# Kernel tuning notes

Measured on AMD Instinct MI355X. Metric: run time of the kernel, lower is better.

Reference implementation:

```python
import jax, jax.numpy as jnp
import numpy as np

N_HEAD = 16
D_MODEL = 1024
D_HEAD = D_MODEL // N_HEAD
B, T = 2, 2048


def setup_inputs() -> dict:
    key = jax.random.key(0)
    k1, k2, k3 = jax.random.split(key, 3)
    x = jax.random.normal(k1, (B, T, D_MODEL), dtype=jnp.float32)
    w_attn = jax.random.normal(k2, (3 * D_MODEL, D_MODEL), dtype=jnp.float32) * (D_MODEL ** -0.5)
    w_proj = jax.random.normal(k3, (D_MODEL, D_MODEL), dtype=jnp.float32) * (D_MODEL ** -0.5)
    return {"x": x, "w_attn": w_attn, "w_proj": w_proj}


def _rms_norm(x):
    eps = jnp.asarray(jnp.finfo(x.dtype).eps, x.dtype)
    var = jnp.mean(jnp.square(x), axis=-1, keepdims=True)
    return x * jax.lax.rsqrt(var + eps)


def _rotate_half(x):
    x1, x2 = jnp.split(x, 2, axis=-1)
    return jnp.concatenate((-x2, x1), axis=-1)


def reference(x, w_attn, w_proj):
    Bx, Tx, C = x.shape
    qkv = jnp.einsum('btc,fc->btf', x, w_attn)  # [B,T,3C]
    q, k, v = jnp.split(qkv, 3, axis=-1)
    # [B, H, T, Dh]
    q = q.reshape(Bx, Tx, N_HEAD, D_HEAD).transpose(0, 2, 1, 3)
    k = k.reshape(Bx, Tx, N_HEAD, D_HEAD).transpose(0, 2, 1, 3)
    v = v.reshape(Bx, Tx, N_HEAD, D_HEAD).transpose(0, 2, 1, 3)
    # QK RMSNorm (no learned weight)
    q = _rms_norm(q)
    k = _rms_norm(k)
    # Rotary embedding over full d_head: freqs tiled twice
    inv_freq = 1.0 / (10000.0 ** (jnp.arange(0, D_HEAD, 2, dtype=jnp.float32) / D_HEAD))
    t = jnp.arange(Tx, dtype=jnp.float32)
    freqs = jnp.einsum('i,j->ij', t, inv_freq)  # [T, Dh/2]
    emb = jnp.concatenate((freqs, freqs), axis=-1)  # [T, Dh]
    cos = jnp.cos(emb)[None, None, :, :]
    sin = jnp.sin(emb)[None, None, :, :]
    q = q * cos + _rotate_half(q) * sin
    k = k * cos + _rotate_half(k) * sin
    # Causal SDPA
    scale = D_HEAD ** -0.5
    scores = jnp.einsum('bhqd,bhkd->bhqk', q, k) * scale
    causal = jnp.tril(jnp.ones((Tx, Tx), dtype=bool))
    scores = jnp.where(causal[None, None], scores, jnp.asarray(-jnp.inf, scores.dtype))
    attn = jax.nn.softmax(scores, axis=-1)
    y = jnp.einsum('bhqk,bhkd->bhqd', attn, v)
    y = y.transpose(0, 2, 1, 3).reshape(Bx, Tx, C)
    return jnp.einsum('btc,oc->bto', y, w_proj)
```

## Files before the change

kernel.cpp:

```cpp
#include <hip/hip_runtime.h>
#include <cstdint>
#include <cstddef>


typedef short bf16x8 __attribute__((ext_vector_type(8)));
typedef float floatx4 __attribute__((ext_vector_type(4)));
typedef unsigned short ushortx8 __attribute__((ext_vector_type(8)));
typedef unsigned short ushortx4 __attribute__((ext_vector_type(4)));
typedef unsigned int uintx2 __attribute__((ext_vector_type(2)));

#define DEVI __device__ __forceinline__

DEVI float bf2f(unsigned short u) {
    unsigned int x = ((unsigned int)u) << 16;
    return __builtin_bit_cast(float, x);
}
DEVI unsigned short f2bf(float f) {
    unsigned int u = __builtin_bit_cast(unsigned int, f);
    u += 0x7fffu + ((u >> 16) & 1u);
    return (unsigned short)(u >> 16);
}
DEVI unsigned int pkbf2(float a, float b) {
    unsigned int ua = __builtin_bit_cast(unsigned int, a) + 0x8000u;
    unsigned int ub = __builtin_bit_cast(unsigned int, b) + 0x8000u;
    return __builtin_amdgcn_perm(ub, ua, 0x07060302);
}

DEVI void glds16(const unsigned short* g, unsigned short* l) {
    __builtin_amdgcn_global_load_lds(
        (const __attribute__((address_space(1))) unsigned int*)g,
        (__attribute__((address_space(3))) unsigned int*)l, 16, 0, 0);
}

DEVI void cast8(unsigned short* dst, const float* src) {
    floatx4 a = *(const floatx4*)src;
    floatx4 b = *(const floatx4*)(src + 4);
    ushortx8 o;
    o[0] = f2bf(a[0]); o[1] = f2bf(a[1]); o[2] = f2bf(a[2]); o[3] = f2bf(a[3]);
    o[4] = f2bf(b[0]); o[5] = f2bf(b[1]); o[6] = f2bf(b[2]); o[7] = f2bf(b[3]);
    *(ushortx8*)dst = o;
}

__global__ __launch_bounds__(256)
void cast_inputs(const float* __restrict__ x, const float* __restrict__ wa,
                 const float* __restrict__ wp,
                 unsigned short* __restrict__ xb, unsigned short* __restrict__ wab,
                 unsigned short* __restrict__ wpb)
{
    size_t g = (size_t)blockIdx.x * 256 + threadIdx.x;
    size_t stride = (size_t)gridDim.x * 256;
    for (size_t i = g; i < (4194304 / 8); i += stride) cast8(xb  + i * 8, x  + i * 8);
    for (size_t i = g; i < (3145728 / 8); i += stride) cast8(wab + i * 8, wa + i * 8);
    for (size_t i = g; i < (1048576 / 8); i += stride) cast8(wpb + i * 8, wp + i * 8);
}

template <bool QKV_SPLIT, int BN, int BK>
__global__ __launch_bounds__(256)
void gemm_bt(const unsigned short* __restrict__ A, const unsigned short* __restrict__ B,
             unsigned short* __restrict__ Cqk, float* __restrict__ Cf,
             unsigned short* __restrict__ Vt, int M, int N, int K)
{
    constexpr int WCOLS = (BN == 128) ? 2 : 1;
    constexpr int WROWS = 4 / WCOLS;
    constexpr int MI    = 128 / (16 * WROWS);
    constexpr int LPR   = BK / 8;
    constexpr int RPI   = 64 / LPR;

    __shared__ __align__(16) unsigned short As[128 * BK];
    __shared__ __align__(16) unsigned short Bs[BN * BK];

    const int tid  = threadIdx.x;
    const int lane = tid & 63;
    const int w    = tid >> 6;
    const int wm   = w / WCOLS, wn = w % WCOLS;
    const int quad = lane >> 4;
    const int lm   = lane & 15;
    const int m0 = blockIdx.y * 128;
    const int n0 = blockIdx.x * BN;
    const int sr = lane / LPR;
    const int sc = (lane % LPR) * 8;

    floatx4 acc[MI][4] = {};

    for (int k0 = 0; k0 < K; k0 += BK) {
        __syncthreads();
        #pragma unroll
        for (int i = 0; i < 32 / RPI; ++i) {
            int r = w * 32 + i * RPI;
            glds16(&A[(size_t)(m0 + r + sr) * K + k0 + sc], &As[r * BK]);
        }
        #pragma unroll
        for (int i = 0; i < (BN / 4) / RPI; ++i) {
            int r = w * (BN / 4) + i * RPI;
            glds16(&B[(size_t)(n0 + r + sr) * K + k0 + sc], &Bs[r * BK]);
        }
        __syncthreads();

        #pragma unroll
        for (int kk = 0; kk < BK / 32; ++kk) {
            bf16x8 a[MI];
            #pragma unroll
            for (int i = 0; i < MI; ++i)
                a[i] = *(const bf16x8*)&As[(wm * (16 * MI) + i * 16 + lm) * BK + kk * 32 + quad * 8];
            #pragma unroll
            for (int j = 0; j < 4; ++j) {
                bf16x8 b = *(const bf16x8*)&Bs[(wn * 64 + j * 16 + lm) * BK + kk * 32 + quad * 8];
                #pragma unroll
                for (int i = 0; i < MI; ++i)
                    acc[i][j] = __builtin_amdgcn_mfma_f32_16x16x32_bf16(a[i], b, acc[i][j], 0, 0, 0);
            }
        }
    }

    if constexpr (QKV_SPLIT) {
        const bool is_v = (n0 + wn * 64) >= 2048;
        if (!is_v) {
            float rn[MI][4];
            #pragma unroll
            for (int i = 0; i < MI; ++i)
                #pragma unroll
                for (int r = 0; r < 4; ++r) {
                    float s = 0.0f;
                    #pragma unroll
                    for (int j = 0; j < 4; ++j) s += acc[i][j][r] * acc[i][j][r];
                    s += __shfl_xor(s, 1, 64);
                    s += __shfl_xor(s, 2, 64);
                    s += __shfl_xor(s, 4, 64);
                    s += __shfl_xor(s, 8, 64);
                    rn[i][r] = rsqrtf(s * (1.0f / 64.0f) + 1.1920929e-07f);
                }
            float invf[4];
            #pragma unroll
            for (int j = 0; j < 4; ++j) {
                int d = j * 16 + lm;
                invf[j] = __expf(-(float)(d & 31) * 0.28782313662425572f);
            }
            #pragma unroll
            for (int i = 0; i < MI; ++i)
                #pragma unroll
                for (int r = 0; r < 4; ++r) {
                    int row = m0 + wm * (16 * MI) + i * 16 + quad * 4 + r;
                    float t = (float)(row & 2047);
                    float g = rn[i][r];
                    #pragma unroll
                    for (int j = 0; j < 4; ++j) {
                        int d = j * 16 + lm;
                        float sn, cs;
                        __sincosf(t * invf[j], &sn, &cs);
                        float v  = acc[i][j][r] * g;
                        float vp = acc[i][j ^ 2][r] * g;
                        float sgn = (d < 32) ? -1.0f : 1.0f;
                        Cqk[(size_t)row * 2048 + (n0 + wn * 64 + d)] =
                            f2bf(v * cs + sgn * vp * sn);
                    }
                }
        } else {
            #pragma unroll
            for (int i = 0; i < MI; ++i)
                #pragma unroll
                for (int j = 0; j < 4; ++j) {
                    int col  = n0 + wn * 64 + j * 16 + lm;
                    int row0 = m0 + wm * (16 * MI) + i * 16 + quad * 4;
                    int bq = row0 >> 11, t0 = row0 & 2047;
                    ushortx4 pk;
                    #pragma unroll
                    for (int r = 0; r < 4; ++r) pk[r] = f2bf(acc[i][j][r]);
                    *(ushortx4*)&Vt[((size_t)(bq * 1024 + (col - 2048))) * 2048 + t0] = pk;
                }
        }
    } else {
        #pragma unroll
        for (int i = 0; i < MI; ++i)
            #pragma unroll
            for (int j = 0; j < 4; ++j) {
                int col  = n0 + wn * 64 + j * 16 + lm;
                int row0 = m0 + wm * (16 * MI) + i * 16 + quad * 4;
                #pragma unroll
                for (int r = 0; r < 4; ++r)
                    Cf[(size_t)(row0 + r) * N + col] = acc[i][j][r];
            }
    }
}

#define ATTN_STEP(KSc, VSc, KSn, VSn, KT, DG, LAST)                            \
  do {                                                                         \
    if (!(LAST)) {                                                             \
      *(ushortx8*)&(KSn)[r0 * LD + pc] = kreg0;                                \
      *(ushortx8*)&(KSn)[r1 * LD + pc] = kreg1;                                \
      *(ushortx8*)&(VSn)[r0 * LD + pc] = vreg0;                                \
      *(ushortx8*)&(VSn)[r1 * LD + pc] = vreg1;                                \
      if ((KT) + 2 <= qt) {                                                    \
        kreg0 = *(const ushortx8*)kp0; kreg1 = *(const ushortx8*)kp1;          \
        vreg0 = *(const ushortx8*)vp0; vreg1 = *(const ushortx8*)vp1;          \
        kp0 += (size_t)64 * 2048; kp1 += (size_t)64 * 2048;                    \
        vp0 += 64; vp1 += 64;                                                  \
      }                                                                        \
    }                                                                          \
    floatx4 sa[4] = {};                                                        \
    _Pragma("unroll")                                                          \
    for (int kk = 0; kk < 2; ++kk)                                             \
      _Pragma("unroll")                                                        \
      for (int j = 0; j < 4; ++j) {                                            \
        bf16x8 kf = *(const bf16x8*)&(KSc)[(j * 16 + lm) * LD + kk * 32 + quad * 8]; \
        sa[j] = __builtin_amdgcn_mfma_f32_16x16x32_bf16(kf, qf[kk], sa[j], 0, 0, 0); \
      }                                                                        \
    _Pragma("unroll")                                                          \
    for (int j = 0; j < 4; ++j) {                                              \
      float p0 = exp2f(sa[j][0] * c1 - c2);                                    \
      float p1 = exp2f(sa[j][1] * c1 - c2);                                    \
      float p2 = exp2f(sa[j][2] * c1 - c2);                                    \
      float p3 = exp2f(sa[j][3] * c1 - c2);                                    \
      if (DG) {                                                                \
        int kb = (KT) * 64 + j * 16 + quad * 4;                                \
        if (kb + 0 > qrow) p0 = 0.0f;                                          \
        if (kb + 1 > qrow) p1 = 0.0f;                                          \
        if (kb + 2 > qrow) p2 = 0.0f;                                          \
        if (kb + 3 > qrow) p3 = 0.0f;                                          \
      }                                                                        \
      uintx2 pk;                                                               \
      pk[0] = pkbf2(p0, p1);                                                   \
      pk[1] = pkbf2(p2, p3);                                                   \
      *(uintx2*)&QPs[(w * 16 + lm) * LD + j * 16 + quad * 4] = pk;             \
    }                                                                          \
    _Pragma("unroll")                                                          \
    for (int kk = 0; kk < 2; ++kk) {                                           \
      bf16x8 pf = *(const bf16x8*)&QPs[(w * 16 + lm) * LD + kk * 32 + quad * 8]; \
      _Pragma("unroll")                                                        \
      for (int j = 0; j < 4; ++j) {                                            \
        bf16x8 vf = *(const bf16x8*)&(VSc)[(j * 16 + lm) * LD + kk * 32 + quad * 8]; \
        o[j] = __builtin_amdgcn_mfma_f32_16x16x32_bf16(pf, vf, o[j], 0, 0, 0); \
      }                                                                        \
      l_acc = __builtin_amdgcn_mfma_f32_16x16x32_bf16(pf, ones, l_acc, 0, 0, 0); \
    }                                                                          \
    if (!(LAST)) __syncthreads();                                              \
  } while (0)

__global__ __launch_bounds__(256)
void attention(const unsigned short* __restrict__ qk,
               const unsigned short* __restrict__ Vt,
               unsigned short* __restrict__ Y)
{
    constexpr int LD = 72;
    __shared__ __align__(16) unsigned short QPs[64 * LD];
    __shared__ __align__(16) unsigned short Ks0[64 * LD];
    __shared__ __align__(16) unsigned short Ks1[64 * LD];
    __shared__ __align__(16) unsigned short Vs0[64 * LD];
    __shared__ __align__(16) unsigned short Vs1[64 * LD];

    const int tid  = threadIdx.x;
    const int lane = tid & 63;
    const int w    = tid >> 6;
    const int quad = lane >> 4;
    const int lm   = lane & 15;

    const int bh = blockIdx.x;
    const int qt = 31 - blockIdx.y;
    const int b  = bh >> 4, h = bh & 15;
    const int q0 = qt * 64;
    const int qrow = q0 + w * 16 + lm;

    const int r0 = tid >> 3, r1 = r0 + 32, pc = (tid & 7) * 8;
    const unsigned short* kp0 = qk + (size_t)b * 2048 * 2048 + 1024 + h * 64
                              + (size_t)r0 * 2048 + pc;
    const unsigned short* kp1 = kp0 + (size_t)32 * 2048;
    const unsigned short* vp0 = Vt + (size_t)bh * 64 * 2048 + (size_t)r0 * 2048 + pc;
    const unsigned short* vp1 = vp0 + (size_t)32 * 2048;

    #pragma unroll
    for (int i = 0; i < 2; ++i) {
        int c = i * 256 + tid, row = c >> 3, col = (c & 7) * 8;
        *(ushortx8*)&QPs[row * LD + col] =
            *(const ushortx8*)&qk[((size_t)(b * 2048 + q0 + row)) * 2048 + h * 64 + col];
    }

    ushortx8 kreg0 = *(const ushortx8*)kp0, kreg1 = *(const ushortx8*)kp1;
    ushortx8 vreg0 = *(const ushortx8*)vp0, vreg1 = *(const ushortx8*)vp1;
    kp0 += (size_t)64 * 2048; kp1 += (size_t)64 * 2048;
    vp0 += 64; vp1 += 64;
    *(ushortx8*)&Ks0[r0 * LD + pc] = kreg0;
    *(ushortx8*)&Ks0[r1 * LD + pc] = kreg1;
    *(ushortx8*)&Vs0[r0 * LD + pc] = vreg0;
    *(ushortx8*)&Vs0[r1 * LD + pc] = vreg1;
    if (qt >= 1) {
        kreg0 = *(const ushortx8*)kp0; kreg1 = *(const ushortx8*)kp1;
        vreg0 = *(const ushortx8*)vp0; vreg1 = *(const ushortx8*)vp1;
        kp0 += (size_t)64 * 2048; kp1 += (size_t)64 * 2048;
        vp0 += 64; vp1 += 64;
    }
    __syncthreads();

    bf16x8 qf[2];
    #pragma unroll
    for (int kk = 0; kk < 2; ++kk)
        qf[kk] = *(const bf16x8*)&QPs[(w * 16 + lm) * LD + kk * 32 + quad * 8];

    bf16x8 ones;
    #pragma unroll
    for (int i = 0; i < 8; ++i) ones[i] = (short)0x3F80;

    floatx4 o[4] = {};
    floatx4 l_acc = {};
    const float c1 = 0.125f * 1.44269504f;
    const float c2 = 8.0f   * 1.44269504f;

    int kt = 0;
    for (; kt + 1 < qt; kt += 2) {
        ATTN_STEP(Ks0, Vs0, Ks1, Vs1, kt,     false, false);
        ATTN_STEP(Ks1, Vs1, Ks0, Vs0, kt + 1, false, false);
    }
    if (kt < qt) {
        ATTN_STEP(Ks0, Vs0, Ks1, Vs1, kt, false, false);
        ATTN_STEP(Ks1, Vs1, Ks0, Vs0, qt, true, true);
    } else {
        ATTN_STEP(Ks0, Vs0, Ks1, Vs1, qt, true, true);
    }

    float rinv[4];
    #pragma unroll
    for (int r = 0; r < 4; ++r) rinv[r] = 1.0f / l_acc[r];

    #pragma unroll
    for (int j = 0; j < 4; ++j) {
        int colg = h * 64 + j * 16 + lm;
        #pragma unroll
        for (int r = 0; r < 4; ++r) {
            int rowg = q0 + w * 16 + quad * 4 + r;
            Y[((size_t)(b * 2048 + rowg)) * 1024 + colg] = f2bf(o[j][r] * rinv[r]);
        }
    }
}

extern "C" void kernel_launch(void* const* d_in, const int* in_sizes, int n_in,
                              void* d_out, int out_size, void* d_ws, size_t ws_size,
                              hipStream_t stream)
{
    const float* x      = (const float*)d_in[0];
    const float* w_attn = (const float*)d_in[1];
    const float* w_proj = (const float*)d_in[2];
    float* out = (float*)d_out;

    unsigned short* qkbuf = (unsigned short*)d_ws;
    unsigned short* Vtb   = qkbuf + (size_t)4096 * 2048;
    unsigned short* y     = Vtb   + (size_t)32 * 64 * 2048;
    unsigned short* wpb   = y     + (size_t)4096 * 1024;
    unsigned short* xb  = (unsigned short*)d_out;
    unsigned short* wab = xb + (size_t)4096 * 1024;

    dim3 blk(256);
    cast_inputs<<<dim3(1024), blk, 0, stream>>>(x, w_attn, w_proj, xb, wab, wpb);
    gemm_bt<true, 128, 32>
        <<<dim3(24, 32), blk, 0, stream>>>(xb, wab, qkbuf, nullptr, Vtb, 4096, 3072, 1024);
    attention<<<dim3(32, 32), blk, 0, stream>>>(qkbuf, Vtb, y);
    gemm_bt<false, 64, 64>
        <<<dim3(16, 32), blk, 0, stream>>>(y, wpb, nullptr, out, nullptr, 4096, 1024, 1024);
}
```

Measured before the change: 177.3 us.

## Replace QKV GEMM with 256x256 eight-phase pipelined kernel using direct LDS loads

```diff
diff --git a/kernel.cpp b/kernel.cpp
--- a/kernel.cpp
+++ b/kernel.cpp
@@ -52,6 +52,178 @@
     for (size_t i = g; i < (4194304 / 8); i += stride) cast8(xb  + i * 8, x  + i * 8);
     for (size_t i = g; i < (3145728 / 8); i += stride) cast8(wab + i * 8, wa + i * 8);
     for (size_t i = g; i < (1048576 / 8); i += stride) cast8(wpb + i * 8, wp + i * 8);
+}
+
+__global__ __launch_bounds__(512, 2)
+void gemm_qkv_8ph(const unsigned short* __restrict__ A,
+                  const unsigned short* __restrict__ B,
+                  unsigned short* __restrict__ Cqk,
+                  unsigned short* __restrict__ Vt)
+{
+    __shared__ __align__(16) unsigned short lds[2][2][256 * 64];
+
+    const int tid  = threadIdx.x;
+    const int lane = tid & 63;
+    const int w    = tid >> 6;
+    const int wm   = w >> 2;
+    const int wn   = w & 3;
+    const int quad = lane >> 4;
+    const int lm   = lane & 15;
+
+    const int lin = blockIdx.y * 12 + blockIdx.x;
+    const int s   = (lin & 7) * 24 + (lin >> 3);
+    const int m0  = (s / 12) * 256;
+    const int n0  = (s % 12) * 256;
+
+    const int srow = tid >> 3;
+    const int scol = ((tid & 7) * 8) ^ (((tid >> 5) & 1) << 4);
+    const int ldst = w * 512;
+
+#define STG_A(u, WBi, kq) glds16(&A[(size_t)(m0 + (u) * 64 + srow) * 1024 + (kq) + scol], \
+                                 &lds[WBi][0][(u) * 4096 + ldst])
+#define STG_B(u, WBi, kq) glds16(&B[(size_t)(n0 + (u) * 64 + srow) * 1024 + (kq) + scol], \
+                                 &lds[WBi][1][(u) * 4096 + ldst])
+#define RD_A(RBi, rrow, off) (*(const bf16x8*)&lds[RBi][0][(((rrow) * 64 + (off))) ^ ((((rrow) >> 2) & 1) << 4)])
+#define RD_B(RBi, rrow, off) (*(const bf16x8*)&lds[RBi][1][(((rrow) * 64 + (off))) ^ ((((rrow) >> 2) & 1) << 4)])
+
+    floatx4 acc[8][4] = {};
+    bf16x8 afr[4][2];
+    bf16x8 bfr[4][2];
+
+#define MQ(MB, JB)                                                              \
+  do {                                                                          \
+    _Pragma("unroll")                                                           \
+    for (int kk = 0; kk < 2; ++kk)                                              \
+      _Pragma("unroll")                                                         \
+      for (int mi = 0; mi < 4; ++mi)                                            \
+        _Pragma("unroll")                                                       \
+        for (int j2 = 0; j2 < 2; ++j2)                                          \
+          acc[(MB) + mi][(JB) + j2] = __builtin_amdgcn_mfma_f32_16x16x32_bf16(  \
+              afr[mi][kk], bfr[(JB) + j2][kk], acc[(MB) + mi][(JB) + j2], 0, 0, 0); \
+  } while (0)
+
+#define TILE(RBi, WBi, KT, LASTF)                                               \
+  do {                                                                          \
+    const int kn = ((KT) + 1) * 64;                                             \
+               \
+    _Pragma("unroll")                                                           \
+    for (int kk = 0; kk < 2; ++kk) {                                            \
+      _Pragma("unroll")                                                         \
+      for (int mi = 0; mi < 4; ++mi)                                            \
+        afr[mi][kk] = RD_A(RBi, wm * 128 + mi * 16 + lm, kk * 32 + quad * 8);   \
+      _Pragma("unroll")                                                         \
+      for (int j2 = 0; j2 < 2; ++j2)                                            \
+        bfr[j2][kk] = RD_B(RBi, wn * 64 + j2 * 16 + lm, kk * 32 + quad * 8);    \
+    }                                                                           \
+    if (!(LASTF)) { STG_B(0, WBi, kn); STG_B(1, WBi, kn); }                     \
+    __builtin_amdgcn_s_barrier();                                               \
+    asm volatile("s_waitcnt lgkmcnt(0)" ::: "memory");                          \
+    __builtin_amdgcn_s_setprio(1); MQ(0, 0); __builtin_amdgcn_s_setprio(0);     \
+    __builtin_amdgcn_s_barrier();                                               \
+              \
+    _Pragma("unroll")                                                           \
+    for (int kk = 0; kk < 2; ++kk)                                              \
+      _Pragma("unroll")                                                         \
+      for (int j2 = 0; j2 < 2; ++j2)                                            \
+        bfr[2 + j2][kk] = RD_B(RBi, wn * 64 + (2 + j2) * 16 + lm, kk * 32 + quad * 8); \
+    if (!(LASTF)) { STG_B(2, WBi, kn); STG_B(3, WBi, kn);                       \
+                    asm volatile("s_waitcnt vmcnt(4)" ::: "memory"); }          \
+    else          { asm volatile("s_waitcnt vmcnt(0)" ::: "memory"); }          \
+    __builtin_amdgcn_s_barrier();                                               \
+    asm volatile("s_waitcnt lgkmcnt(0)" ::: "memory");                          \
+    __builtin_amdgcn_s_setprio(1); MQ(0, 2); __builtin_amdgcn_s_setprio(0);     \
+    __builtin_amdgcn_s_barrier();                                               \
+                          \
+    _Pragma("unroll")                                                           \
+    for (int kk = 0; kk < 2; ++kk)                                              \
+      _Pragma("unroll")                                                         \
+      for (int mi = 0; mi < 4; ++mi)                                            \
+        afr[mi][kk] = RD_A(RBi, wm * 128 + 64 + mi * 16 + lm, kk * 32 + quad * 8); \
+    if (!(LASTF)) { STG_A(0, WBi, kn); STG_A(2, WBi, kn); }                     \
+    __builtin_amdgcn_s_barrier();                                               \
+    asm volatile("s_waitcnt lgkmcnt(0)" ::: "memory");                          \
+    __builtin_amdgcn_s_setprio(1); MQ(4, 2); __builtin_amdgcn_s_setprio(0);     \
+    __builtin_amdgcn_s_barrier();                                               \
+      \
+    if (!(LASTF)) { STG_A(1, WBi, kn); STG_A(3, WBi, kn);                       \
+                    asm volatile("s_waitcnt vmcnt(2)" ::: "memory"); }          \
+    __builtin_amdgcn_s_barrier();                                               \
+    __builtin_amdgcn_s_setprio(1); MQ(4, 0); __builtin_amdgcn_s_setprio(0);     \
+    __builtin_amdgcn_s_barrier();                                               \
+  } while (0)
+
+    STG_B(0, 0, 0); STG_B(1, 0, 0); STG_B(2, 0, 0); STG_B(3, 0, 0);
+    STG_A(0, 0, 0); STG_A(2, 0, 0); STG_A(1, 0, 0); STG_A(3, 0, 0);
+    asm volatile("s_waitcnt vmcnt(2)" ::: "memory");
+    __builtin_amdgcn_s_barrier();
+
+    for (int kt = 0; kt < 14; kt += 2) {
+        TILE(0, 1, kt, false);
+        TILE(1, 0, kt + 1, false);
+    }
+    TILE(0, 1, 14, false);
+    TILE(1, 0, 15, true);
+
+    const bool is_v = (n0 + wn * 64) >= 2048;
+    if (!is_v) {
+        float invf[4];
+        #pragma unroll
+        for (int j = 0; j < 4; ++j) {
+            int d = j * 16 + lm;
+            invf[j] = __expf(-(float)(d & 31) * 0.28782313662425572f);
+        }
+        #pragma unroll
+        for (int mi = 0; mi < 8; ++mi) {
+            float rn[4];
+            #pragma unroll
+            for (int r = 0; r < 4; ++r) {
+                float ss = 0.0f;
+                #pragma unroll
+                for (int j = 0; j < 4; ++j) ss += acc[mi][j][r] * acc[mi][j][r];
+                ss += __shfl_xor(ss, 1, 64);
+                ss += __shfl_xor(ss, 2, 64);
+                ss += __shfl_xor(ss, 4, 64);
+                ss += __shfl_xor(ss, 8, 64);
+                rn[r] = rsqrtf(ss * (1.0f / 64.0f) + 1.1920929e-07f);
+            }
+            #pragma unroll
+            for (int r = 0; r < 4; ++r) {
+                int row = m0 + wm * 128 + mi * 16 + quad * 4 + r;
+                float t = (float)(row & 2047);
+                float g = rn[r];
+                #pragma unroll
+                for (int j = 0; j < 4; ++j) {
+                    int d = j * 16 + lm;
+                    float sn, cs;
+                    __sincosf(t * invf[j], &sn, &cs);
+                    float v  = acc[mi][j][r] * g;
+                    float vp = acc[mi][j ^ 2][r] * g;
+                    float sgn = (d < 32) ? -1.0f : 1.0f;
+                    Cqk[(size_t)row * 2048 + (n0 + wn * 64 + d)] =
+                        f2bf(v * cs + sgn * vp * sn);
+                }
+            }
+        }
+    } else {
+        #pragma unroll
+        for (int mi = 0; mi < 8; ++mi)
+            #pragma unroll
+            for (int j = 0; j < 4; ++j) {
+                int col  = n0 + wn * 64 + j * 16 + lm;
+                int row0 = m0 + wm * 128 + mi * 16 + quad * 4;
+                int bq = row0 >> 11, t0 = row0 & 2047;
+                ushortx4 pk;
+                #pragma unroll
+                for (int r = 0; r < 4; ++r) pk[r] = f2bf(acc[mi][j][r]);
+                *(ushortx4*)&Vt[((size_t)(bq * 1024 + (col - 2048))) * 2048 + t0] = pk;
+            }
+    }
+#undef TILE
+#undef MQ
+#undef RD_A
+#undef RD_B
+#undef STG_A
+#undef STG_B
 }
 
 template <bool QKV_SPLIT, int BN, int BK>
@@ -348,8 +520,7 @@
 
     dim3 blk(256);
     cast_inputs<<<dim3(1024), blk, 0, stream>>>(x, w_attn, w_proj, xb, wab, wpb);
-    gemm_bt<true, 128, 32>
-        <<<dim3(24, 32), blk, 0, stream>>>(xb, wab, qkbuf, nullptr, Vtb, 4096, 3072, 1024);
+    gemm_qkv_8ph<<<dim3(12, 16), dim3(512), 0, stream>>>(xb, wab, qkbuf, Vtb);
     attention<<<dim3(32, 32), blk, 0, stream>>>(qkbuf, Vtb, y);
     gemm_bt<false, 64, 64>
         <<<dim3(16, 32), blk, 0, stream>>>(y, wpb, nullptr, out, nullptr, 4096, 1024, 1024);
```

Result: slower. 185.5 us (+4.7%).
